# Optimization experiments

Measured on AMD Instinct MI355X. Metric: run time of the kernel, lower is better.

## Reference

```python
import jax, jax.numpy as jnp
import numpy as np

H = 512; W = 512
NUM_CLS = 3; NUM_ANCH = 6; CODE = 7
DIR_BINS = 2; DIR_OFFSET = 0.78539; DIR_LIMIT_OFFSET = 0.0
SCORE_THRESH = 0.1; PRE_K = 4096; POST_K = 500; IOU_THRESH = 0.01
N = H * W * NUM_ANCH  # 1,572,864 anchors


def make_anchors():
    # grid anchors matching [H, W, 3 classes, 2 rotations, 7] layout -> [N, 7]
    xs = jnp.linspace(0.0, 69.12, W, dtype=jnp.float32)
    ys = jnp.linspace(-39.68, 39.68, H, dtype=jnp.float32)
    yy, xx = jnp.meshgrid(ys, xs, indexing='ij')
    cen = jnp.stack([xx, yy, jnp.full_like(xx, -1.0)], -1)  # [H,W,3]
    sizes = jnp.array([[3.9, 1.6, 1.56], [0.8, 0.6, 1.73], [1.76, 0.6, 1.73]], jnp.float32)
    rots = jnp.array([0.0, np.pi / 2], jnp.float32)
    cen = jnp.broadcast_to(cen[:, :, None, None, :], (H, W, 3, 2, 3))
    siz = jnp.broadcast_to(sizes[None, None, :, None, :], (H, W, 3, 2, 3))
    rot = jnp.broadcast_to(rots[None, None, None, :, None], (H, W, 3, 2, 1))
    return jnp.concatenate([cen, siz, rot], -1).reshape(N, CODE)


def setup_inputs() -> dict:
    key = jax.random.key(0)
    k1, k2, k3 = jax.random.split(key, 3)
    return {
        'cls_preds': jax.random.normal(k1, (1, H, W, NUM_ANCH * NUM_CLS), jnp.float32),
        'box_preds': jax.random.normal(k2, (1, H, W, NUM_ANCH * CODE), jnp.float32),
        'dir_cls_preds': jax.random.normal(k3, (1, H, W, NUM_ANCH * DIR_BINS), jnp.float32),
        'anchors': make_anchors(),
    }


def decode_boxes(box_preds, anchors):
    # OpenPCDet ResidualCoder.decode_torch
    xa, ya, za, dxa, dya, dza, ra = [anchors[:, i] for i in range(CODE)]
    xt, yt, zt, dxt, dyt, dzt, rt = [box_preds[:, i] for i in range(CODE)]
    za = za + dza * 0.5
    diag = jnp.sqrt(dxa * dxa + dya * dya)
    xg = xt * diag + xa
    yg = yt * diag + ya
    zg = zt * dza + za
    dxg = jnp.exp(dxt) * dxa
    dyg = jnp.exp(dyt) * dya
    dzg = jnp.exp(dzt) * dza
    rg = rt + ra
    zg = zg - dzg * 0.5
    return jnp.stack([xg, yg, zg, dxg, dyg, dzg, rg], -1)


def reference(cls_preds, box_preds, dir_cls_preds, anchors):
    cls = cls_preds.reshape(N, NUM_CLS)
    box = box_preds.reshape(N, CODE)
    dirp = dir_cls_preds.reshape(N, DIR_BINS)
    boxes = decode_boxes(box, anchors)  # [N,7]
    # direction classifier: limit_period then add bin offset
    dir_labels = jnp.argmax(dirp, -1).astype(jnp.float32)
    period = 2.0 * np.pi / DIR_BINS
    rot = boxes[:, 6]
    val = rot - DIR_OFFSET
    val = val - jnp.floor(val / period + DIR_LIMIT_OFFSET) * period
    rot = val + DIR_OFFSET + period * dir_labels
    boxes = jnp.concatenate([boxes[:, :6], rot[:, None]], -1)
    # post_processing: sigmoid scores, class-agnostic NMS
    probs = jax.nn.sigmoid(cls)
    scores = probs.max(-1)
    labels = probs.argmax(-1) + 1
    scores = jnp.where(scores >= SCORE_THRESH, scores, 0.0)
    top_scores, top_idx = jax.lax.top_k(scores, PRE_K)
    tb = boxes[top_idx]  # [PRE_K,7]
    tl = labels[top_idx]
    # axis-aligned BEV IoU (rotation-agnostic approximation of rotated NMS)
    x1 = tb[:, 0] - tb[:, 3] * 0.5; x2 = tb[:, 0] + tb[:, 3] * 0.5
    y1 = tb[:, 1] - tb[:, 4] * 0.5; y2 = tb[:, 1] + tb[:, 4] * 0.5
    area = (x2 - x1) * (y2 - y1)
    ix = jnp.clip(jnp.minimum(x2[:, None], x2[None, :]) - jnp.maximum(x1[:, None], x1[None, :]), 0.0)
    iy = jnp.clip(jnp.minimum(y2[:, None], y2[None, :]) - jnp.maximum(y1[:, None], y1[None, :]), 0.0)
    inter = ix * iy
    iou = inter / (area[:, None] + area[None, :] - inter + 1e-6)  # [PRE_K,PRE_K]
    valid = top_scores > 0.0
    idxs = jnp.arange(PRE_K)
    def step(keep, i):
        row = iou[i]
        suppressed = jnp.any((row > IOU_THRESH) & keep & (idxs < i))
        ki = valid[i] & jnp.logical_not(suppressed)
        return keep.at[i].set(ki), None
    keep, _ = jax.lax.scan(step, jnp.zeros(PRE_K, bool), idxs)
    final_scores = jnp.where(keep, top_scores, 0.0)
    fs, fi = jax.lax.top_k(final_scores, POST_K)
    out = jnp.concatenate([tb[fi], fs[:, None]], -1)  # [POST_K, 8] boxes+score
    return out, tl[fi]
```

## Files before the change

### kernel.cpp

```cpp
#include <hip/hip_runtime.h>
#include <math.h>

namespace {
constexpr int H = 512, W = 512, NUM_ANCH = 6;
constexpr int N = H * W * NUM_ANCH;
constexpr int NG = N / 4;
constexpr int PREK = 4096;
constexpr int POSTK = 500;
constexpr float SCORE_THRESH = 0.1f;
constexpr float IOU_THRESH = 0.01f;
constexpr float DIR_OFFSET = 0.78539f;
constexpr float PERIOD = 3.14159265358979323846f;
constexpr int LISTB_CAP = 8192;

constexpr size_t oScores = 0;
constexpr size_t oMask   = 0;
constexpr size_t oDiag2  = (size_t)PREK * 64 * 8;
constexpr size_t oHist12 = (size_t)N * 4;
constexpr size_t oHistA  = oHist12 + 4096 * 4;
constexpr size_t oHistB  = oHistA + 1024 * 4;
constexpr size_t oMeta   = oHistB + 1024 * 4;
constexpr size_t oListAS = oMeta + 64 * 4;
constexpr size_t oListAI = oListAS + PREK * 4;
constexpr size_t oListB  = oListAI + PREK * 4;
constexpr size_t oTopS   = oListB + (size_t)LISTB_CAP * 4;
constexpr size_t oTopI   = oTopS + PREK * 4;
constexpr size_t oTB     = oTopI + PREK * 4;
constexpr size_t oB4     = oTB + (size_t)PREK * 7 * 4;
constexpr size_t oLabel  = oB4 + (size_t)PREK * 16;
constexpr size_t oValidW = oLabel + PREK * 4;
constexpr size_t WS_NEED = oValidW + 64 * 8;
}

__device__ __forceinline__ float sigmoid_rn(float x) {
  return (float)(1.0 / (1.0 + exp(-(double)x)));
}

__device__ __forceinline__ unsigned long long rdl64(unsigned long long v, int src) {
  unsigned lo = (unsigned)__builtin_amdgcn_readlane((int)(unsigned)v, src);
  unsigned hi = (unsigned)__builtin_amdgcn_readlane((int)(unsigned)(v >> 32), src);
  return ((unsigned long long)hi << 32) | lo;
}

__device__ __forceinline__ unsigned long long rl2(unsigned lo, unsigned hi, int ln) {
  unsigned a = (unsigned)__builtin_amdgcn_readlane((int)lo, ln);
  unsigned b = (unsigned)__builtin_amdgcn_readlane((int)hi, ln);
  return ((unsigned long long)b << 32) | a;
}

__device__ __forceinline__ void scan_find(const unsigned* __restrict__ hist, int nbins,
                                          unsigned R, unsigned& bin, unsigned& above,
                                          unsigned* part) {
  int t = threadIdx.x;
  int chunk = nbins >> 8;
  unsigned s = 0;
  for (int c = 0; c < chunk; ++c) s += hist[t * chunk + c];
  part[t] = s;
  __syncthreads();
  for (int off = 1; off < 256; off <<= 1) {
    unsigned v = part[t];
    unsigned add = (t + off < 256) ? part[t + off] : 0u;
    __syncthreads();
    part[t] = v + add;
    __syncthreads();
  }
  unsigned cum = (t == 255) ? 0u : part[t + 1];
  for (int c = chunk - 1; c >= 0; --c) {
    unsigned hv = hist[t * chunk + c];
    unsigned ab = cum;
    cum += hv;
    if (cum >= R && ab < R) { part[256] = (unsigned)(t * chunk + c); part[257] = ab; }
  }
  __syncthreads();
  bin = part[256];
  above = part[257];
  __syncthreads();
}

__global__ __launch_bounds__(256) void k_scores(const float4* __restrict__ cls4,
                                                float4* __restrict__ scores4,
                                                unsigned* __restrict__ hist12) {
  __shared__ unsigned h[4096];
  for (int t = threadIdx.x; t < 4096; t += 256) h[t] = 0;
  __syncthreads();
  int stride = gridDim.x * 256;
  for (int g = blockIdx.x * 256 + threadIdx.x; g < NG; g += stride) {
    float4 a = cls4[(size_t)g * 3 + 0];
    float4 b = cls4[(size_t)g * 3 + 1];
    float4 c = cls4[(size_t)g * 3 + 2];
    float m0 = fmaxf(a.x, fmaxf(a.y, a.z));
    float m1 = fmaxf(a.w, fmaxf(b.x, b.y));
    float m2 = fmaxf(b.z, fmaxf(b.w, c.x));
    float m3 = fmaxf(c.y, fmaxf(c.z, c.w));
    float s0 = sigmoid_rn(m0); s0 = (s0 >= SCORE_THRESH) ? s0 : 0.0f;
    float s1 = sigmoid_rn(m1); s1 = (s1 >= SCORE_THRESH) ? s1 : 0.0f;
    float s2 = sigmoid_rn(m2); s2 = (s2 >= SCORE_THRESH) ? s2 : 0.0f;
    float s3 = sigmoid_rn(m3); s3 = (s3 >= SCORE_THRESH) ? s3 : 0.0f;
    scores4[g] = make_float4(s0, s1, s2, s3);
    atomicAdd(&h[__float_as_uint(s0) >> 20], 1u);
    atomicAdd(&h[__float_as_uint(s1) >> 20], 1u);
    atomicAdd(&h[__float_as_uint(s2) >> 20], 1u);
    atomicAdd(&h[__float_as_uint(s3) >> 20], 1u);
  }
  __syncthreads();
  for (int t = threadIdx.x; t < 4096; t += 256) {
    unsigned v = h[t];
    if (v) atomicAdd(&hist12[t], v);
  }
}

__global__ __launch_bounds__(256) void k_refineA(const float4* __restrict__ scores4,
                                                 const unsigned* __restrict__ hist12,
                                                 unsigned* __restrict__ histA,
                                                 unsigned* __restrict__ meta) {
  __shared__ unsigned h[1024];
  __shared__ unsigned part[258];
  for (int t = threadIdx.x; t < 1024; t += 256) h[t] = 0;
  unsigned T1, ab1;
  scan_find(hist12, 4096, PREK, T1, ab1, part);
  if (threadIdx.x == 0) { meta[0] = T1; meta[1] = ab1; }
  int stride = gridDim.x * 256;
  for (int g = blockIdx.x * 256 + threadIdx.x; g < NG; g += stride) {
    float4 s = scores4[g];
    unsigned bb[4] = {__float_as_uint(s.x), __float_as_uint(s.y),
                      __float_as_uint(s.z), __float_as_uint(s.w)};
#pragma unroll
    for (int k = 0; k < 4; ++k)
      if ((bb[k] >> 20) == T1) atomicAdd(&h[(bb[k] >> 10) & 1023u], 1u);
  }
  __syncthreads();
  for (int t = threadIdx.x; t < 1024; t += 256) {
    unsigned v = h[t];
    if (v) atomicAdd(&histA[t], v);
  }
}

__global__ __launch_bounds__(256) void k_refineB(const float4* __restrict__ scores4,
                                                 const unsigned* __restrict__ histA,
                                                 unsigned* __restrict__ histB,
                                                 unsigned* __restrict__ meta) {
  __shared__ unsigned h[1024];
  __shared__ unsigned part[258];
  for (int t = threadIdx.x; t < 1024; t += 256) h[t] = 0;
  unsigned m0 = meta[0], prev = meta[1];
  unsigned T2, ab2;
  scan_find(histA, 1024, PREK - prev, T2, ab2, part);
  if (threadIdx.x == 0) { meta[2] = T2; meta[3] = prev + ab2; }
  unsigned pref22 = (m0 << 10) | T2;
  int stride = gridDim.x * 256;
  for (int g = blockIdx.x * 256 + threadIdx.x; g < NG; g += stride) {
    float4 s = scores4[g];
    unsigned bb[4] = {__float_as_uint(s.x), __float_as_uint(s.y),
                      __float_as_uint(s.z), __float_as_uint(s.w)};
#pragma unroll
    for (int k = 0; k < 4; ++k)
      if ((bb[k] >> 10) == pref22) atomicAdd(&h[bb[k] & 1023u], 1u);
  }
  __syncthreads();
  for (int t = threadIdx.x; t < 1024; t += 256) {
    unsigned v = h[t];
    if (v) atomicAdd(&histB[t], v);
  }
}

__global__ __launch_bounds__(256) void k_compactS(const float4* __restrict__ scores4,
                                                  const unsigned* __restrict__ histB,
                                                  unsigned* __restrict__ meta,
                                                  float* __restrict__ laS,
                                                  unsigned* __restrict__ laI,
                                                  unsigned* __restrict__ lb) {
  __shared__ unsigned part[258];
  unsigned m0 = meta[0], m2 = meta[2], prev = meta[3];
  unsigned R3 = PREK - prev;
  unsigned T3, ab3;
  scan_find(histB, 1024, R3, T3, ab3, part);
  if (threadIdx.x == 0) { meta[12] = T3; meta[6] = R3 - ab3; }
  unsigned thr = (m0 << 20) | (m2 << 10) | T3;
  int stride = gridDim.x * 256;
  for (int g = blockIdx.x * 256 + threadIdx.x; g < NG; g += stride) {
    float4 s = scores4[g];
    float sv[4] = {s.x, s.y, s.z, s.w};
#pragma unroll
    for (int k = 0; k < 4; ++k) {
      unsigned bits = __float_as_uint(sv[k]);
      int n = g * 4 + k;
      if (bits > thr) {
        unsigned pos = atomicAdd(&meta[7], 1u);
        if (pos < (unsigned)PREK) { laS[pos] = sv[k]; laI[pos] = (unsigned)n; }
      } else if (bits == thr) {
        unsigned pos = atomicAdd(&meta[8], 1u);
        if (pos < (unsigned)LISTB_CAP) lb[pos] = (unsigned)n;
      }
    }
  }
}

__global__ __launch_bounds__(1024) void k_select(const unsigned* __restrict__ meta,
                                                 const float* __restrict__ laS,
                                                 const unsigned* __restrict__ laI,
                                                 const unsigned* __restrict__ lb,
                                                 float* __restrict__ topS,
                                                 unsigned* __restrict__ topI,
                                                 unsigned long long* __restrict__ validW) {
  __shared__ unsigned arrB[LISTB_CAP];
  __shared__ unsigned long long arr[PREK];
  int t = threadIdx.x;
  unsigned E = meta[6];
  unsigned G = meta[7];
  unsigned cntB = meta[8];
  if (cntB > (unsigned)LISTB_CAP) cntB = LISTB_CAP;
  unsigned thr = (meta[0] << 20) | (meta[2] << 10) | meta[12];

  if (E != 0) {
    int n2 = 2;
    while ((unsigned)n2 < cntB) n2 <<= 1;
    for (int i = t; i < n2; i += 1024) arrB[i] = (i < (int)cntB) ? lb[i] : 0xFFFFFFFFu;
    __syncthreads();
    if (cntB != E) {
      for (int k = 2; k <= n2; k <<= 1) {
        for (int j = k >> 1; j > 0; j >>= 1) {
          for (int p = t; p < n2 / 2; p += 1024) {
            int i = ((p / j) * (2 * j)) + (p % j);
            int l = i + j;
            bool up = ((i & k) == 0);
            unsigned a = arrB[i], b = arrB[l];
            if ((a > b) == up) { arrB[i] = b; arrB[l] = a; }
          }
          __syncthreads();
        }
      }
    }
    for (int i = t; i < (int)E; i += 1024)
      arr[G + i] = ((unsigned long long)thr << 32) | (unsigned long long)(~arrB[i]);
  }
  __syncthreads();
  for (int i = t; i < PREK; i += 1024)
    if (i < (int)G)
      arr[i] = ((unsigned long long)__float_as_uint(laS[i]) << 32) |
               (unsigned long long)(~laI[i]);
  __syncthreads();
  for (int k = 2; k <= PREK; k <<= 1) {
    for (int j = k >> 1; j > 0; j >>= 1) {
      for (int p = t; p < PREK / 2; p += 1024) {
        int i = ((p / j) * (2 * j)) + (p % j);
        int l = i + j;
        bool up = ((i & k) == 0);
        unsigned long long a = arr[i], b = arr[l];
        if ((a < b) == up) { arr[i] = b; arr[l] = a; }
      }
      __syncthreads();
    }
  }
  for (int i = t; i < PREK; i += 1024) {
    unsigned long long key = arr[i];
    unsigned sb = (unsigned)(key >> 32);
    topS[i] = __uint_as_float(sb);
    topI[i] = ~((unsigned)key);
    unsigned long long bal = __ballot(sb != 0);
    if ((t & 63) == 0) validW[i >> 6] = bal;
  }
}

__global__ void k_decode(const float* __restrict__ cls, const float* __restrict__ box,
                         const float* __restrict__ dir, const float* __restrict__ anc,
                         const unsigned* __restrict__ topI,
                         float* __restrict__ tb, float4* __restrict__ b4,
                         unsigned* __restrict__ label) {
  int i = blockIdx.x * blockDim.x + threadIdx.x;
  if (i >= PREK) return;
  size_t idx = (size_t)topI[i];
  const float* a = anc + idx * 7;
  const float* b = box + idx * 7;
  float xa = a[0], ya = a[1], za = a[2], dxa = a[3], dya = a[4], dza = a[5], ra = a[6];
  float xt = b[0], yt = b[1], zt = b[2], dxt = b[3], dyt = b[4], dzt = b[5], rt = b[6];
  za = za + dza * 0.5f;
  float diagl = sqrtf(dxa * dxa + dya * dya);
  float xg = xt * diagl + xa;
  float yg = yt * diagl + ya;
  float zg = zt * dza + za;
  float dxg = (float)exp((double)dxt) * dxa;
  float dyg = (float)exp((double)dyt) * dya;
  float dzg = (float)exp((double)dzt) * dza;
  float rg = rt + ra;
  zg = zg - dzg * 0.5f;
  float d0 = dir[idx * 2], d1 = dir[idx * 2 + 1];
  float dl = (d1 > d0) ? 1.0f : 0.0f;
  float val = rg - DIR_OFFSET;
  val = val - floorf(val / PERIOD) * PERIOD;
  float rot = val + DIR_OFFSET + PERIOD * dl;
  float l0 = cls[idx * 3 + 0];
  float l1 = cls[idx * 3 + 1];
  float l2 = cls[idx * 3 + 2];
  unsigned lab = 1;
  float bestl = l0;
  if (l1 > bestl) { bestl = l1; lab = 2; }
  if (l2 > bestl) { bestl = l2; lab = 3; }
  tb[i * 7 + 0] = xg; tb[i * 7 + 1] = yg; tb[i * 7 + 2] = zg;
  tb[i * 7 + 3] = dxg; tb[i * 7 + 4] = dyg; tb[i * 7 + 5] = dzg;
  tb[i * 7 + 6] = rot;
  float X1 = xg - dxg * 0.5f, X2 = xg + dxg * 0.5f;
  float Y1 = yg - dyg * 0.5f, Y2 = yg + dyg * 0.5f;
  b4[i] = make_float4(X1, Y1, X2, Y2);
  label[i] = lab;
}

__global__ __launch_bounds__(256) void k_maskgen(const float4* __restrict__ b4,
                                                 unsigned long long* __restrict__ mask,
                                                 unsigned long long* __restrict__ diag2) {
  __shared__ float4 sb[PREK];
  int t = threadIdx.x;
  for (int i = t; i < PREK; i += 256) sb[i] = b4[i];
  __syncthreads();
  int lane = t & 63, wv = t >> 6;
  for (int k = wv; k < 16; k += 4) {
    int r = blockIdx.x + (k << 8);
    float4 bi = sb[r];
    float A = (bi.z - bi.x) * (bi.w - bi.y);
    unsigned long long myword = 0;
    unsigned long long d0 = 0, d1 = 0;
    int w0 = r >> 6;
    int b2 = (r >> 7) << 1;
    for (int w = w0; w < 64; ++w) {
      int j = (w << 6) + lane;
      float4 bj = sb[j];
      float ix = fminf(bi.z, bj.z) - fmaxf(bi.x, bj.x); ix = fmaxf(ix, 0.0f);
      float iy = fminf(bi.w, bj.w) - fmaxf(bi.y, bj.y); iy = fmaxf(iy, 0.0f);
      float inter = ix * iy;
      float Aj = (bj.z - bj.x) * (bj.w - bj.y);
      float iou = inter / (A + Aj - inter + 1e-6f);
      unsigned long long word = __ballot(j > r && iou > IOU_THRESH);
      if (lane == w) myword = word;
      if (w == b2) d0 = word;
      if (w == b2 + 1) d1 = word;
    }
    mask[((size_t)r << 6) + lane] = myword;
    if (lane == 0) {
      unsigned long long* dp = diag2 +
          ((size_t)(r >> 7) * 256 + (size_t)((r >> 6) & 1) * 128 + (size_t)(r & 63) * 2);
      dp[0] = d0; dp[1] = d1;
    }
  }
}

__global__ __launch_bounds__(512) void k_tail(const float* __restrict__ topS,
                                              const float* __restrict__ tb,
                                              const unsigned* __restrict__ label,
                                              const unsigned long long* __restrict__ validW,
                                              const unsigned long long* __restrict__ mask,
                                              const unsigned long long* __restrict__ diag2,
                                              float* __restrict__ out) {
  __shared__ unsigned long long kwS[64];
  __shared__ int part[512];
  __shared__ short keptList[PREK];
  __shared__ short nonKept[PREK];
  int t = threadIdx.x;
  if (t < 64) {
    int lane = t;
    unsigned long long valid_l = validW[lane];
    unsigned long long removed = 0, keep_l = 0;
    const uint4* d4 = (const uint4*)diag2;
    uint4 dA = d4[lane];
    uint4 dB = d4[64 + lane];
    int keptTotal = 0;
    for (int c = 0; c < 32; ++c) {
      uint4 dA1 = dA, dB1 = dB;
      if (c + 1 < 32) {
        dA1 = d4[(c + 1) * 128 + lane];
        dB1 = d4[(c + 1) * 128 + 64 + lane];
      }
      unsigned long long rem0 = rdl64(removed, 2 * c);
      unsigned long long rem1 = rdl64(removed, 2 * c + 1);
      unsigned long long val0 = rdl64(valid_l, 2 * c);
      unsigned long long val1 = rdl64(valid_l, 2 * c + 1);
      unsigned long long p0 = val0 & ~rem0;
      unsigned long long p1 = val1 & ~rem1;
      unsigned long long k0 = 0, k1 = 0;
      while (p0) {
        int b = __ffsll((long long)p0) - 1;
        b = __builtin_amdgcn_readfirstlane(b);
        k0 |= (1ull << b);
        unsigned long long r0 = rl2(dA.x, dA.y, b);
        unsigned long long r1 = rl2(dA.z, dA.w, b);
        p0 &= (p0 - 1);
        p0 &= ~r0;
        p1 &= ~r1;
      }
      while (p1) {
        int b = __ffsll((long long)p1) - 1;
        b = __builtin_amdgcn_readfirstlane(b);
        k1 |= (1ull << b);
        unsigned long long r1 = rl2(dB.z, dB.w, b);
        p1 &= (p1 - 1);
        p1 &= ~r1;
      }
      if (lane == 2 * c) keep_l = k0;
      if (lane == 2 * c + 1) keep_l = k1;
      keptTotal += (int)__popcll(k0) + (int)__popcll(k1);
      if (keptTotal >= POSTK) break;
      unsigned long long kw0 = k0, kw1 = k1;
      size_t rowbase = ((size_t)c << 7);
      while (kw0 | kw1) {
        unsigned long long vv[16];
        unsigned long long mk[16];
#pragma unroll
        for (int u = 0; u < 16; ++u) {
          bool en = ((kw0 | kw1) != 0);
          int b = 0;
          if (kw0) { b = __ffsll((long long)kw0) - 1; kw0 &= kw0 - 1; }
          else if (kw1) { b = 64 + __ffsll((long long)kw1) - 1; kw1 &= kw1 - 1; }
          mk[u] = en ? ~0ull : 0ull;
          vv[u] = mask[((rowbase + (size_t)b) << 6) + lane];
        }
        unsigned long long o = 0;
#pragma unroll
        for (int u = 0; u < 16; ++u) o |= (vv[u] & mk[u]);
        removed |= o;
      }
      dA = dA1;
      dB = dB1;
    }
    kwS[lane] = keep_l;
  }
  __syncthreads();
  int base = t * 8;
  int cnt = 0;
  for (int e = 0; e < 8; ++e) {
    int i = base + e;
    cnt += (int)((kwS[i >> 6] >> (i & 63)) & 1ull);
  }
  part[t] = cnt;
  __syncthreads();
  for (int off = 1; off < 512; off <<= 1) {
    int v = part[t];
    int add = (t >= off) ? part[t - off] : 0;
    __syncthreads();
    part[t] = v + add;
    __syncthreads();
  }
  int kbase = part[t] - cnt;
  int nbase = base - kbase;
  for (int e = 0; e < 8; ++e) {
    int i = base + e;
    bool kp = ((kwS[i >> 6] >> (i & 63)) & 1ull) != 0;
    if (kp) keptList[kbase++] = (short)i;
    else nonKept[nbase++] = (short)i;
  }
  __syncthreads();
  int keptCount = part[511];
  for (int k = t; k < POSTK; k += 512) {
    int i;
    float s;
    if (k < keptCount) { i = keptList[k]; s = topS[i]; }
    else { i = nonKept[k - keptCount]; s = 0.0f; }
    for (int c = 0; c < 7; ++c) out[k * 8 + c] = tb[i * 7 + c];
    out[k * 8 + 7] = s;
    out[POSTK * 8 + k] = (float)label[i];
  }
}

extern "C" void kernel_launch(void* const* d_in, const int* in_sizes, int n_in,
                              void* d_out, int out_size, void* d_ws, size_t ws_size,
                              hipStream_t stream) {
  const float* cls = (const float*)d_in[0];
  const float* box = (const float*)d_in[1];
  const float* dir = (const float*)d_in[2];
  const float* anc = (const float*)d_in[3];
  float* out = (float*)d_out;
  char* ws = (char*)d_ws;
  if (ws_size < WS_NEED) return;

  float* scores = (float*)(ws + oScores);
  unsigned* hist12 = (unsigned*)(ws + oHist12);
  unsigned* histA = (unsigned*)(ws + oHistA);
  unsigned* histB = (unsigned*)(ws + oHistB);
  unsigned* meta = (unsigned*)(ws + oMeta);
  float* laS = (float*)(ws + oListAS);
  unsigned* laI = (unsigned*)(ws + oListAI);
  unsigned* lb = (unsigned*)(ws + oListB);
  float* topS = (float*)(ws + oTopS);
  unsigned* topI = (unsigned*)(ws + oTopI);
  float* tb = (float*)(ws + oTB);
  float4* b4 = (float4*)(ws + oB4);
  unsigned* label = (unsigned*)(ws + oLabel);
  unsigned long long* validW = (unsigned long long*)(ws + oValidW);
  unsigned long long* mask = (unsigned long long*)(ws + oMask);
  unsigned long long* diag2 = (unsigned long long*)(ws + oDiag2);

  hipMemsetAsync(ws + oHist12, 0, (oListAS - oHist12), stream);

  k_scores<<<256, 256, 0, stream>>>((const float4*)cls, (float4*)scores, hist12);
  k_refineA<<<256, 256, 0, stream>>>((const float4*)scores, hist12, histA, meta);
  k_refineB<<<256, 256, 0, stream>>>((const float4*)scores, histA, histB, meta);
  k_compactS<<<256, 256, 0, stream>>>((const float4*)scores, histB, meta, laS, laI, lb);
  k_select<<<1, 1024, 0, stream>>>(meta, laS, laI, lb, topS, topI, validW);
  k_decode<<<PREK / 256, 256, 0, stream>>>(cls, box, dir, anc, topI, tb, b4, label);
  k_maskgen<<<256, 256, 0, stream>>>(b4, mask, diag2);
  k_tail<<<1, 512, 0, stream>>>(topS, tb, label, validW, mask, diag2, out);
}
```

Before: 220.3 us.

## Compact top-bucket candidates once and refine top-k in a single block with fused decode

Replaces two extra full-array histogram passes and a separate compaction with one compaction of all scores in or above the first-level threshold bucket into a 64K candidate buffer. The second and third radix refinement levels, the tie handling and the final sort then run inside one 1024-thread block over that buffer. Box decoding is fused into the same kernel, removing two launches and the topI round trip. The risk is that the candidate bucket may exceed the fixed capacity and the single-block refinement serialises work over many candidates.

```diff
diff --git a/kernel.cpp b/kernel.cpp
--- a/kernel.cpp
+++ b/kernel.cpp
@@ -7,25 +7,22 @@
 constexpr int NG = N / 4;
 constexpr int PREK = 4096;
 constexpr int POSTK = 500;
+constexpr int CAP2 = 65536;
+constexpr int TIEC = 8184;
 constexpr float SCORE_THRESH = 0.1f;
 constexpr float IOU_THRESH = 0.01f;
 constexpr float DIR_OFFSET = 0.78539f;
 constexpr float PERIOD = 3.14159265358979323846f;
-constexpr int LISTB_CAP = 8192;
 
 constexpr size_t oScores = 0;
 constexpr size_t oMask   = 0;
 constexpr size_t oDiag2  = (size_t)PREK * 64 * 8;
 constexpr size_t oHist12 = (size_t)N * 4;
-constexpr size_t oHistA  = oHist12 + 4096 * 4;
-constexpr size_t oHistB  = oHistA + 1024 * 4;
-constexpr size_t oMeta   = oHistB + 1024 * 4;
-constexpr size_t oListAS = oMeta + 64 * 4;
-constexpr size_t oListAI = oListAS + PREK * 4;
-constexpr size_t oListB  = oListAI + PREK * 4;
-constexpr size_t oTopS   = oListB + (size_t)LISTB_CAP * 4;
-constexpr size_t oTopI   = oTopS + PREK * 4;
-constexpr size_t oTB     = oTopI + PREK * 4;
+constexpr size_t oMeta   = oHist12 + 4096 * 4;
+constexpr size_t oCandS  = oMeta + 256;
+constexpr size_t oCandI  = oCandS + (size_t)CAP2 * 4;
+constexpr size_t oTopS   = oCandI + (size_t)CAP2 * 4;
+constexpr size_t oTB     = oTopS + PREK * 4;
 constexpr size_t oB4     = oTB + (size_t)PREK * 7 * 4;
 constexpr size_t oLabel  = oB4 + (size_t)PREK * 16;
 constexpr size_t oValidW = oLabel + PREK * 4;
@@ -109,73 +106,16 @@
   }
 }
 
-__global__ __launch_bounds__(256) void k_refineA(const float4* __restrict__ scores4,
-                                                 const unsigned* __restrict__ hist12,
-                                                 unsigned* __restrict__ histA,
-                                                 unsigned* __restrict__ meta) {
-  __shared__ unsigned h[1024];
+__global__ __launch_bounds__(256) void k_compact2(const float4* __restrict__ scores4,
+                                                  const unsigned* __restrict__ hist12,
+                                                  unsigned* __restrict__ meta,
+                                                  float* __restrict__ caS,
+                                                  unsigned* __restrict__ caI) {
   __shared__ unsigned part[258];
-  for (int t = threadIdx.x; t < 1024; t += 256) h[t] = 0;
   unsigned T1, ab1;
   scan_find(hist12, 4096, PREK, T1, ab1, part);
   if (threadIdx.x == 0) { meta[0] = T1; meta[1] = ab1; }
-  int stride = gridDim.x * 256;
-  for (int g = blockIdx.x * 256 + threadIdx.x; g < NG; g += stride) {
-    float4 s = scores4[g];
-    unsigned bb[4] = {__float_as_uint(s.x), __float_as_uint(s.y),
-                      __float_as_uint(s.z), __float_as_uint(s.w)};
-#pragma unroll
-    for (int k = 0; k < 4; ++k)
-      if ((bb[k] >> 20) == T1) atomicAdd(&h[(bb[k] >> 10) & 1023u], 1u);
-  }
-  __syncthreads();
-  for (int t = threadIdx.x; t < 1024; t += 256) {
-    unsigned v = h[t];
-    if (v) atomicAdd(&histA[t], v);
-  }
-}
-
-__global__ __launch_bounds__(256) void k_refineB(const float4* __restrict__ scores4,
-                                                 const unsigned* __restrict__ histA,
-                                                 unsigned* __restrict__ histB,
-                                                 unsigned* __restrict__ meta) {
-  __shared__ unsigned h[1024];
-  __shared__ unsigned part[258];
-  for (int t = threadIdx.x; t < 1024; t += 256) h[t] = 0;
-  unsigned m0 = meta[0], prev = meta[1];
-  unsigned T2, ab2;
-  scan_find(histA, 1024, PREK - prev, T2, ab2, part);
-  if (threadIdx.x == 0) { meta[2] = T2; meta[3] = prev + ab2; }
-  unsigned pref22 = (m0 << 10) | T2;
-  int stride = gridDim.x * 256;
-  for (int g = blockIdx.x * 256 + threadIdx.x; g < NG; g += stride) {
-    float4 s = scores4[g];
-    unsigned bb[4] = {__float_as_uint(s.x), __float_as_uint(s.y),
-                      __float_as_uint(s.z), __float_as_uint(s.w)};
-#pragma unroll
-    for (int k = 0; k < 4; ++k)
-      if ((bb[k] >> 10) == pref22) atomicAdd(&h[bb[k] & 1023u], 1u);
-  }
-  __syncthreads();
-  for (int t = threadIdx.x; t < 1024; t += 256) {
-    unsigned v = h[t];
-    if (v) atomicAdd(&histB[t], v);
-  }
-}
-
-__global__ __launch_bounds__(256) void k_compactS(const float4* __restrict__ scores4,
-                                                  const unsigned* __restrict__ histB,
-                                                  unsigned* __restrict__ meta,
-                                                  float* __restrict__ laS,
-                                                  unsigned* __restrict__ laI,
-                                                  unsigned* __restrict__ lb) {
-  __shared__ unsigned part[258];
-  unsigned m0 = meta[0], m2 = meta[2], prev = meta[3];
-  unsigned R3 = PREK - prev;
-  unsigned T3, ab3;
-  scan_find(histB, 1024, R3, T3, ab3, part);
-  if (threadIdx.x == 0) { meta[12] = T3; meta[6] = R3 - ab3; }
-  unsigned thr = (m0 << 20) | (m2 << 10) | T3;
+  unsigned lo = T1 << 20;
   int stride = gridDim.x * 256;
   for (int g = blockIdx.x * 256 + threadIdx.x; g < NG; g += stride) {
     float4 s = scores4[g];
@@ -183,40 +123,110 @@
 #pragma unroll
     for (int k = 0; k < 4; ++k) {
       unsigned bits = __float_as_uint(sv[k]);
-      int n = g * 4 + k;
-      if (bits > thr) {
-        unsigned pos = atomicAdd(&meta[7], 1u);
-        if (pos < (unsigned)PREK) { laS[pos] = sv[k]; laI[pos] = (unsigned)n; }
-      } else if (bits == thr) {
-        unsigned pos = atomicAdd(&meta[8], 1u);
-        if (pos < (unsigned)LISTB_CAP) lb[pos] = (unsigned)n;
-      }
-    }
-  }
-}
-
-__global__ __launch_bounds__(1024) void k_select(const unsigned* __restrict__ meta,
-                                                 const float* __restrict__ laS,
-                                                 const unsigned* __restrict__ laI,
-                                                 const unsigned* __restrict__ lb,
-                                                 float* __restrict__ topS,
-                                                 unsigned* __restrict__ topI,
-                                                 unsigned long long* __restrict__ validW) {
-  __shared__ unsigned arrB[LISTB_CAP];
+      if (bits >= lo) {
+        unsigned pos = atomicAdd(&meta[9], 1u);
+        if (pos < (unsigned)CAP2) { caS[pos] = sv[k]; caI[pos] = (unsigned)(g * 4 + k); }
+      }
+    }
+  }
+}
+
+__global__ __launch_bounds__(1024) void k_select2(const unsigned* __restrict__ meta,
+                                                  const float* __restrict__ caS,
+                                                  const unsigned* __restrict__ caI,
+                                                  const float* __restrict__ cls,
+                                                  const float* __restrict__ box,
+                                                  const float* __restrict__ dir,
+                                                  const float* __restrict__ anc,
+                                                  float* __restrict__ topS,
+                                                  unsigned long long* __restrict__ validW,
+                                                  float* __restrict__ tb,
+                                                  float4* __restrict__ b4,
+                                                  unsigned* __restrict__ label) {
   __shared__ unsigned long long arr[PREK];
+  __shared__ unsigned arrB[TIEC];
+  __shared__ unsigned sres[8];
+  unsigned* h = (unsigned*)arr;
+  unsigned* scan = arrB;
   int t = threadIdx.x;
-  unsigned E = meta[6];
-  unsigned G = meta[7];
-  unsigned cntB = meta[8];
-  if (cntB > (unsigned)LISTB_CAP) cntB = LISTB_CAP;
-  unsigned thr = (meta[0] << 20) | (meta[2] << 10) | meta[12];
-
+  unsigned T1 = meta[0], ab1 = meta[1];
+  unsigned cnt2 = meta[9];
+  if (cnt2 > (unsigned)CAP2) cnt2 = CAP2;
+  h[t] = 0;
+  __syncthreads();
+  for (unsigned i = t; i < cnt2; i += 1024) {
+    unsigned bits = __float_as_uint(caS[i]);
+    if ((bits >> 20) == T1) atomicAdd(&h[(bits >> 10) & 1023u], 1u);
+  }
+  __syncthreads();
+  scan[t] = h[t];
+  __syncthreads();
+  for (int off = 1; off < 1024; off <<= 1) {
+    unsigned v = scan[t];
+    unsigned add = (t + off < 1024) ? scan[t + off] : 0u;
+    __syncthreads();
+    scan[t] = v + add;
+    __syncthreads();
+  }
+  unsigned R2 = PREK - ab1;
+  {
+    unsigned cum = scan[t];
+    unsigned ab = (t == 1023) ? 0u : scan[t + 1];
+    if (cum >= R2 && ab < R2) { sres[0] = (unsigned)t; sres[1] = ab; }
+  }
+  __syncthreads();
+  unsigned T2 = sres[0], ab2 = sres[1];
+  __syncthreads();
+  h[t] = 0;
+  __syncthreads();
+  unsigned pref22 = (T1 << 10) | T2;
+  for (unsigned i = t; i < cnt2; i += 1024) {
+    unsigned bits = __float_as_uint(caS[i]);
+    if ((bits >> 10) == pref22) atomicAdd(&h[bits & 1023u], 1u);
+  }
+  __syncthreads();
+  scan[t] = h[t];
+  __syncthreads();
+  for (int off = 1; off < 1024; off <<= 1) {
+    unsigned v = scan[t];
+    unsigned add = (t + off < 1024) ? scan[t + off] : 0u;
+    __syncthreads();
+    scan[t] = v + add;
+    __syncthreads();
+  }
+  unsigned R3 = R2 - ab2;
+  {
+    unsigned cum = scan[t];
+    unsigned ab = (t == 1023) ? 0u : scan[t + 1];
+    if (cum >= R3 && ab < R3) { sres[2] = (unsigned)t; sres[3] = ab; }
+  }
+  __syncthreads();
+  unsigned T3 = sres[2], ab3 = sres[3];
+  unsigned E = R3 - ab3;
+  unsigned thr = (T1 << 20) | (T2 << 10) | T3;
+  if (t == 0) { sres[4] = 0; sres[5] = 0; }
+  __syncthreads();
+  for (unsigned i = t; i < cnt2; i += 1024) {
+    unsigned bits = __float_as_uint(caS[i]);
+    if (bits > thr) {
+      unsigned pos = atomicAdd(&sres[4], 1u);
+      arr[pos] = ((unsigned long long)bits << 32) | (unsigned long long)(~caI[i]);
+    } else if (bits == thr) {
+      unsigned pos = atomicAdd(&sres[5], 1u);
+      if (pos < (unsigned)TIEC) arrB[pos] = caI[i];
+    }
+  }
+  __syncthreads();
+  unsigned G = sres[4];
+  unsigned cntB = sres[5];
+  if (cntB > (unsigned)TIEC) cntB = TIEC;
   if (E != 0) {
-    int n2 = 2;
-    while ((unsigned)n2 < cntB) n2 <<= 1;
-    for (int i = t; i < n2; i += 1024) arrB[i] = (i < (int)cntB) ? lb[i] : 0xFFFFFFFFu;
-    __syncthreads();
     if (cntB != E) {
+      int n2 = 2;
+      while ((unsigned)n2 < cntB) n2 <<= 1;
+      for (int i = t; i < n2; i += 1024)
+        if (i >= (int)cntB) arrB[i] = 0xFFFFFFFFu;
+      __syncthreads();
       for (int k = 2; k <= n2; k <<= 1) {
         for (int j = k >> 1; j > 0; j >>= 1) {
           for (int p = t; p < n2 / 2; p += 1024) {
@@ -234,11 +244,6 @@
       arr[G + i] = ((unsigned long long)thr << 32) | (unsigned long long)(~arrB[i]);
   }
   __syncthreads();
-  for (int i = t; i < PREK; i += 1024)
-    if (i < (int)G)
-      arr[i] = ((unsigned long long)__float_as_uint(laS[i]) << 32) |
-               (unsigned long long)(~laI[i]);
-  __syncthreads();
   for (int k = 2; k <= PREK; k <<= 1) {
     for (int j = k >> 1; j > 0; j >>= 1) {
       for (int p = t; p < PREK / 2; p += 1024) {
@@ -255,53 +260,43 @@
     unsigned long long key = arr[i];
     unsigned sb = (unsigned)(key >> 32);
     topS[i] = __uint_as_float(sb);
-    topI[i] = ~((unsigned)key);
     unsigned long long bal = __ballot(sb != 0);
     if ((t & 63) == 0) validW[i >> 6] = bal;
-  }
-}
-
-__global__ void k_decode(const float* __restrict__ cls, const float* __restrict__ box,
-                         const float* __restrict__ dir, const float* __restrict__ anc,
-                         const unsigned* __restrict__ topI,
-                         float* __restrict__ tb, float4* __restrict__ b4,
-                         unsigned* __restrict__ label) {
-  int i = blockIdx.x * blockDim.x + threadIdx.x;
-  if (i >= PREK) return;
-  size_t idx = (size_t)topI[i];
-  const float* a = anc + idx * 7;
-  const float* b = box + idx * 7;
-  float xa = a[0], ya = a[1], za = a[2], dxa = a[3], dya = a[4], dza = a[5], ra = a[6];
-  float xt = b[0], yt = b[1], zt = b[2], dxt = b[3], dyt = b[4], dzt = b[5], rt = b[6];
-  za = za + dza * 0.5f;
-  float diagl = sqrtf(dxa * dxa + dya * dya);
-  float xg = xt * diagl + xa;
-  float yg = yt * diagl + ya;
-  float zg = zt * dza + za;
-  float dxg = (float)exp((double)dxt) * dxa;
-  float dyg = (float)exp((double)dyt) * dya;
-  float dzg = (float)exp((double)dzt) * dza;
-  float rg = rt + ra;
-  zg = zg - dzg * 0.5f;
-  float d0 = dir[idx * 2], d1 = dir[idx * 2 + 1];
-  float dl = (d1 > d0) ? 1.0f : 0.0f;
-  float val = rg - DIR_OFFSET;
-  val = val - floorf(val / PERIOD) * PERIOD;
-  float rot = val + DIR_OFFSET + PERIOD * dl;
-  float l0 = cls[idx * 3 + 0];
-  float l1 = cls[idx * 3 + 1];
-  float l2 = cls[idx * 3 + 2];
-  unsigned lab = 1;
-  float bestl = l0;
-  if (l1 > bestl) { bestl = l1; lab = 2; }
-  if (l2 > bestl) { bestl = l2; lab = 3; }
-  tb[i * 7 + 0] = xg; tb[i * 7 + 1] = yg; tb[i * 7 + 2] = zg;
-  tb[i * 7 + 3] = dxg; tb[i * 7 + 4] = dyg; tb[i * 7 + 5] = dzg;
-  tb[i * 7 + 6] = rot;
-  float X1 = xg - dxg * 0.5f, X2 = xg + dxg * 0.5f;
-  float Y1 = yg - dyg * 0.5f, Y2 = yg + dyg * 0.5f;
-  b4[i] = make_float4(X1, Y1, X2, Y2);
-  label[i] = lab;
+    size_t idx = (size_t)(~((unsigned)key));
+    const float* a = anc + idx * 7;
+    const float* b = box + idx * 7;
+    float xa = a[0], ya = a[1], za = a[2], dxa = a[3], dya = a[4], dza = a[5], ra = a[6];
+    float xt = b[0], yt = b[1], zt = b[2], dxt = b[3], dyt = b[4], dzt = b[5], rt = b[6];
+    za = za + dza * 0.5f;
+    float diagl = sqrtf(dxa * dxa + dya * dya);
+    float xg = xt * diagl + xa;
+    float yg = yt * diagl + ya;
+    float zg = zt * dza + za;
+    float dxg = (float)exp((double)dxt) * dxa;
+    float dyg = (float)exp((double)dyt) * dya;
+    float dzg = (float)exp((double)dzt) * dza;
+    float rg = rt + ra;
+    zg = zg - dzg * 0.5f;
+    float d0 = dir[idx * 2], d1 = dir[idx * 2 + 1];
+    float dl = (d1 > d0) ? 1.0f : 0.0f;
+    float val = rg - DIR_OFFSET;
+    val = val - floorf(val / PERIOD) * PERIOD;
+    float rot = val + DIR_OFFSET + PERIOD * dl;
+    float l0 = cls[idx * 3 + 0];
+    float l1 = cls[idx * 3 + 1];
+    float l2 = cls[idx * 3 + 2];
+    unsigned lab = 1;
+    float bestl = l0;
+    if (l1 > bestl) { bestl = l1; lab = 2; }
+    if (l2 > bestl) { bestl = l2; lab = 3; }
+    tb[i * 7 + 0] = xg; tb[i * 7 + 1] = yg; tb[i * 7 + 2] = zg;
+    tb[i * 7 + 3] = dxg; tb[i * 7 + 4] = dyg; tb[i * 7 + 5] = dzg;
+    tb[i * 7 + 6] = rot;
+    float X1 = xg - dxg * 0.5f, X2 = xg + dxg * 0.5f;
+    float Y1 = yg - dyg * 0.5f, Y2 = yg + dyg * 0.5f;
+    b4[i] = make_float4(X1, Y1, X2, Y2);
+    label[i] = lab;
+  }
 }
 
 __global__ __launch_bounds__(256) void k_maskgen(const float4* __restrict__ b4,
@@ -471,14 +466,10 @@
 
   float* scores = (float*)(ws + oScores);
   unsigned* hist12 = (unsigned*)(ws + oHist12);
-  unsigned* histA = (unsigned*)(ws + oHistA);
-  unsigned* histB = (unsigned*)(ws + oHistB);
   unsigned* meta = (unsigned*)(ws + oMeta);
-  float* laS = (float*)(ws + oListAS);
-  unsigned* laI = (unsigned*)(ws + oListAI);
-  unsigned* lb = (unsigned*)(ws + oListB);
+  float* caS = (float*)(ws + oCandS);
+  unsigned* caI = (unsigned*)(ws + oCandI);
   float* topS = (float*)(ws + oTopS);
-  unsigned* topI = (unsigned*)(ws + oTopI);
   float* tb = (float*)(ws + oTB);
   float4* b4 = (float4*)(ws + oB4);
   unsigned* label = (unsigned*)(ws + oLabel);
@@ -486,14 +477,12 @@
   unsigned long long* mask = (unsigned long long*)(ws + oMask);
   unsigned long long* diag2 = (unsigned long long*)(ws + oDiag2);
 
-  hipMemsetAsync(ws + oHist12, 0, (oListAS - oHist12), stream);
+  hipMemsetAsync(ws + oHist12, 0, (oCandS - oHist12), stream);
 
   k_scores<<<256, 256, 0, stream>>>((const float4*)cls, (float4*)scores, hist12);
-  k_refineA<<<256, 256, 0, stream>>>((const float4*)scores, hist12, histA, meta);
-  k_refineB<<<256, 256, 0, stream>>>((const float4*)scores, histA, histB, meta);
-  k_compactS<<<256, 256, 0, stream>>>((const float4*)scores, histB, meta, laS, laI, lb);
-  k_select<<<1, 1024, 0, stream>>>(meta, laS, laI, lb, topS, topI, validW);
-  k_decode<<<PREK / 256, 256, 0, stream>>>(cls, box, dir, anc, topI, tb, b4, label);
+  k_compact2<<<256, 256, 0, stream>>>((const float4*)scores, hist12, meta, caS, caI);
+  k_select2<<<1, 1024, 0, stream>>>(meta, caS, caI, cls, box, dir, anc,
+                                    topS, validW, tb, b4, label);
   k_maskgen<<<256, 256, 0, stream>>>(b4, mask, diag2);
   k_tail<<<1, 512, 0, stream>>>(topS, tb, label, validW, mask, diag2, out);
 }
```

Result: slower. 342.2 us (+55.4%).

## Fuse radix-select passes into one persistent kernel with grid barriers; fold decode into select

Applied to the files above, without the earlier changes.

The four score/histogram/refine/compact kernels are merged into one persistent kernel of 256 blocks that uses a software grid barrier (atomic counter plus phase flag) between the radix-select passes. The thresholds now stay in registers instead of being handed through meta. The separate decode kernel is folded into the single-block select kernel, which drops the topI buffer and two launches. The intent is to remove kernel launch gaps and global round trips. The cost is that the barrier relies on all 256 blocks being co-resident, and decode now runs on a single block instead of 16.

```diff
diff --git a/kernel.cpp b/kernel.cpp
--- a/kernel.cpp
+++ b/kernel.cpp
@@ -7,6 +7,7 @@
 constexpr int NG = N / 4;
 constexpr int PREK = 4096;
 constexpr int POSTK = 500;
+constexpr int FBLK = 256;
 constexpr float SCORE_THRESH = 0.1f;
 constexpr float IOU_THRESH = 0.01f;
 constexpr float DIR_OFFSET = 0.78539f;
@@ -24,8 +25,7 @@
 constexpr size_t oListAI = oListAS + PREK * 4;
 constexpr size_t oListB  = oListAI + PREK * 4;
 constexpr size_t oTopS   = oListB + (size_t)LISTB_CAP * 4;
-constexpr size_t oTopI   = oTopS + PREK * 4;
-constexpr size_t oTB     = oTopI + PREK * 4;
+constexpr size_t oTB     = oTopS + PREK * 4;
 constexpr size_t oB4     = oTB + (size_t)PREK * 7 * 4;
 constexpr size_t oLabel  = oB4 + (size_t)PREK * 16;
 constexpr size_t oValidW = oLabel + PREK * 4;
@@ -46,6 +46,22 @@
   unsigned a = (unsigned)__builtin_amdgcn_readlane((int)lo, ln);
   unsigned b = (unsigned)__builtin_amdgcn_readlane((int)hi, ln);
   return ((unsigned long long)b << 32) | a;
+}
+
+__device__ __forceinline__ void grid_bar(unsigned* cnt, unsigned* phase, unsigned tgt) {
+  __syncthreads();
+  if (threadIdx.x == 0) {
+    unsigned my = __hip_atomic_fetch_add(cnt, 1u, __ATOMIC_ACQ_REL,
+                                         __HIP_MEMORY_SCOPE_AGENT);
+    if (my == (unsigned)(FBLK - 1)) {
+      __hip_atomic_store(cnt, 0u, __ATOMIC_RELAXED, __HIP_MEMORY_SCOPE_AGENT);
+      __hip_atomic_fetch_add(phase, 1u, __ATOMIC_RELEASE, __HIP_MEMORY_SCOPE_AGENT);
+    } else {
+      while (__hip_atomic_load(phase, __ATOMIC_ACQUIRE, __HIP_MEMORY_SCOPE_AGENT) < tgt)
+        __builtin_amdgcn_s_sleep(8);
+    }
+  }
+  __syncthreads();
 }
 
 __device__ __forceinline__ void scan_find(const unsigned* __restrict__ hist, int nbins,
@@ -77,14 +93,24 @@
   __syncthreads();
 }
 
-__global__ __launch_bounds__(256) void k_scores(const float4* __restrict__ cls4,
-                                                float4* __restrict__ scores4,
-                                                unsigned* __restrict__ hist12) {
+__global__ __launch_bounds__(256) void k_front(const float4* __restrict__ cls4,
+                                               float4* __restrict__ scores4,
+                                               unsigned* __restrict__ hist12,
+                                               unsigned* __restrict__ histA,
+                                               unsigned* __restrict__ histB,
+                                               unsigned* __restrict__ meta,
+                                               float* __restrict__ laS,
+                                               unsigned* __restrict__ laI,
+                                               unsigned* __restrict__ lb) {
   __shared__ unsigned h[4096];
-  for (int t = threadIdx.x; t < 4096; t += 256) h[t] = 0;
-  __syncthreads();
-  int stride = gridDim.x * 256;
-  for (int g = blockIdx.x * 256 + threadIdx.x; g < NG; g += stride) {
+  __shared__ unsigned part[258];
+  unsigned* barC = &meta[16];
+  unsigned* barP = &meta[17];
+  int t = threadIdx.x;
+  int stride = FBLK * 256;
+  for (int i = t; i < 4096; i += 256) h[i] = 0;
+  __syncthreads();
+  for (int g = blockIdx.x * 256 + t; g < NG; g += stride) {
     float4 a = cls4[(size_t)g * 3 + 0];
     float4 b = cls4[(size_t)g * 3 + 1];
     float4 c = cls4[(size_t)g * 3 + 2];
@@ -103,24 +129,16 @@
     atomicAdd(&h[__float_as_uint(s3) >> 20], 1u);
   }
   __syncthreads();
-  for (int t = threadIdx.x; t < 4096; t += 256) {
-    unsigned v = h[t];
-    if (v) atomicAdd(&hist12[t], v);
-  }
-}
-
-__global__ __launch_bounds__(256) void k_refineA(const float4* __restrict__ scores4,
-                                                 const unsigned* __restrict__ hist12,
-                                                 unsigned* __restrict__ histA,
-                                                 unsigned* __restrict__ meta) {
-  __shared__ unsigned h[1024];
-  __shared__ unsigned part[258];
-  for (int t = threadIdx.x; t < 1024; t += 256) h[t] = 0;
+  for (int i = t; i < 4096; i += 256) {
+    unsigned v = h[i];
+    if (v) atomicAdd(&hist12[i], v);
+  }
+  grid_bar(barC, barP, 1);
   unsigned T1, ab1;
   scan_find(hist12, 4096, PREK, T1, ab1, part);
-  if (threadIdx.x == 0) { meta[0] = T1; meta[1] = ab1; }
-  int stride = gridDim.x * 256;
-  for (int g = blockIdx.x * 256 + threadIdx.x; g < NG; g += stride) {
+  for (int i = t; i < 1024; i += 256) h[i] = 0;
+  __syncthreads();
+  for (int g = blockIdx.x * 256 + t; g < NG; g += stride) {
     float4 s = scores4[g];
     unsigned bb[4] = {__float_as_uint(s.x), __float_as_uint(s.y),
                       __float_as_uint(s.z), __float_as_uint(s.w)};
@@ -129,26 +147,17 @@
       if ((bb[k] >> 20) == T1) atomicAdd(&h[(bb[k] >> 10) & 1023u], 1u);
   }
   __syncthreads();
-  for (int t = threadIdx.x; t < 1024; t += 256) {
-    unsigned v = h[t];
-    if (v) atomicAdd(&histA[t], v);
-  }
-}
-
-__global__ __launch_bounds__(256) void k_refineB(const float4* __restrict__ scores4,
-                                                 const unsigned* __restrict__ histA,
-                                                 unsigned* __restrict__ histB,
-                                                 unsigned* __restrict__ meta) {
-  __shared__ unsigned h[1024];
-  __shared__ unsigned part[258];
-  for (int t = threadIdx.x; t < 1024; t += 256) h[t] = 0;
-  unsigned m0 = meta[0], prev = meta[1];
+  for (int i = t; i < 1024; i += 256) {
+    unsigned v = h[i];
+    if (v) atomicAdd(&histA[i], v);
+  }
+  grid_bar(barC, barP, 2);
   unsigned T2, ab2;
-  scan_find(histA, 1024, PREK - prev, T2, ab2, part);
-  if (threadIdx.x == 0) { meta[2] = T2; meta[3] = prev + ab2; }
-  unsigned pref22 = (m0 << 10) | T2;
-  int stride = gridDim.x * 256;
-  for (int g = blockIdx.x * 256 + threadIdx.x; g < NG; g += stride) {
+  scan_find(histA, 1024, PREK - ab1, T2, ab2, part);
+  unsigned pref22 = (T1 << 10) | T2;
+  for (int i = t; i < 1024; i += 256) h[i] = 0;
+  __syncthreads();
+  for (int g = blockIdx.x * 256 + t; g < NG; g += stride) {
     float4 s = scores4[g];
     unsigned bb[4] = {__float_as_uint(s.x), __float_as_uint(s.y),
                       __float_as_uint(s.z), __float_as_uint(s.w)};
@@ -157,27 +166,19 @@
       if ((bb[k] >> 10) == pref22) atomicAdd(&h[bb[k] & 1023u], 1u);
   }
   __syncthreads();
-  for (int t = threadIdx.x; t < 1024; t += 256) {
-    unsigned v = h[t];
-    if (v) atomicAdd(&histB[t], v);
-  }
-}
-
-__global__ __launch_bounds__(256) void k_compactS(const float4* __restrict__ scores4,
-                                                  const unsigned* __restrict__ histB,
-                                                  unsigned* __restrict__ meta,
-                                                  float* __restrict__ laS,
-                                                  unsigned* __restrict__ laI,
-                                                  unsigned* __restrict__ lb) {
-  __shared__ unsigned part[258];
-  unsigned m0 = meta[0], m2 = meta[2], prev = meta[3];
-  unsigned R3 = PREK - prev;
+  for (int i = t; i < 1024; i += 256) {
+    unsigned v = h[i];
+    if (v) atomicAdd(&histB[i], v);
+  }
+  grid_bar(barC, barP, 3);
+  unsigned R3 = PREK - ab1 - ab2;
   unsigned T3, ab3;
   scan_find(histB, 1024, R3, T3, ab3, part);
-  if (threadIdx.x == 0) { meta[12] = T3; meta[6] = R3 - ab3; }
-  unsigned thr = (m0 << 20) | (m2 << 10) | T3;
-  int stride = gridDim.x * 256;
-  for (int g = blockIdx.x * 256 + threadIdx.x; g < NG; g += stride) {
+  if (t == 0) {
+    meta[0] = T1; meta[2] = T2; meta[12] = T3; meta[6] = R3 - ab3;
+  }
+  unsigned thr = (T1 << 20) | (T2 << 10) | T3;
+  for (int g = blockIdx.x * 256 + t; g < NG; g += stride) {
     float4 s = scores4[g];
     float sv[4] = {s.x, s.y, s.z, s.w};
 #pragma unroll
@@ -195,13 +196,19 @@
   }
 }
 
-__global__ __launch_bounds__(1024) void k_select(const unsigned* __restrict__ meta,
-                                                 const float* __restrict__ laS,
-                                                 const unsigned* __restrict__ laI,
-                                                 const unsigned* __restrict__ lb,
-                                                 float* __restrict__ topS,
-                                                 unsigned* __restrict__ topI,
-                                                 unsigned long long* __restrict__ validW) {
+__global__ __launch_bounds__(1024) void k_selectdec(const unsigned* __restrict__ meta,
+                                                    const float* __restrict__ laS,
+                                                    const unsigned* __restrict__ laI,
+                                                    const unsigned* __restrict__ lb,
+                                                    const float* __restrict__ cls,
+                                                    const float* __restrict__ box,
+                                                    const float* __restrict__ dir,
+                                                    const float* __restrict__ anc,
+                                                    float* __restrict__ topS,
+                                                    unsigned long long* __restrict__ validW,
+                                                    float* __restrict__ tb,
+                                                    float4* __restrict__ b4,
+                                                    unsigned* __restrict__ label) {
   __shared__ unsigned arrB[LISTB_CAP];
   __shared__ unsigned long long arr[PREK];
   int t = threadIdx.x;
@@ -255,53 +262,43 @@
     unsigned long long key = arr[i];
     unsigned sb = (unsigned)(key >> 32);
     topS[i] = __uint_as_float(sb);
-    topI[i] = ~((unsigned)key);
     unsigned long long bal = __ballot(sb != 0);
     if ((t & 63) == 0) validW[i >> 6] = bal;
-  }
-}
-
-__global__ void k_decode(const float* __restrict__ cls, const float* __restrict__ box,
-                         const float* __restrict__ dir, const float* __restrict__ anc,
-                         const unsigned* __restrict__ topI,
-                         float* __restrict__ tb, float4* __restrict__ b4,
-                         unsigned* __restrict__ label) {
-  int i = blockIdx.x * blockDim.x + threadIdx.x;
-  if (i >= PREK) return;
-  size_t idx = (size_t)topI[i];
-  const float* a = anc + idx * 7;
-  const float* b = box + idx * 7;
-  float xa = a[0], ya = a[1], za = a[2], dxa = a[3], dya = a[4], dza = a[5], ra = a[6];
-  float xt = b[0], yt = b[1], zt = b[2], dxt = b[3], dyt = b[4], dzt = b[5], rt = b[6];
-  za = za + dza * 0.5f;
-  float diagl = sqrtf(dxa * dxa + dya * dya);
-  float xg = xt * diagl + xa;
-  float yg = yt * diagl + ya;
-  float zg = zt * dza + za;
-  float dxg = (float)exp((double)dxt) * dxa;
-  float dyg = (float)exp((double)dyt) * dya;
-  float dzg = (float)exp((double)dzt) * dza;
-  float rg = rt + ra;
-  zg = zg - dzg * 0.5f;
-  float d0 = dir[idx * 2], d1 = dir[idx * 2 + 1];
-  float dl = (d1 > d0) ? 1.0f : 0.0f;
-  float val = rg - DIR_OFFSET;
-  val = val - floorf(val / PERIOD) * PERIOD;
-  float rot = val + DIR_OFFSET + PERIOD * dl;
-  float l0 = cls[idx * 3 + 0];
-  float l1 = cls[idx * 3 + 1];
-  float l2 = cls[idx * 3 + 2];
-  unsigned lab = 1;
-  float bestl = l0;
-  if (l1 > bestl) { bestl = l1; lab = 2; }
-  if (l2 > bestl) { bestl = l2; lab = 3; }
-  tb[i * 7 + 0] = xg; tb[i * 7 + 1] = yg; tb[i * 7 + 2] = zg;
-  tb[i * 7 + 3] = dxg; tb[i * 7 + 4] = dyg; tb[i * 7 + 5] = dzg;
-  tb[i * 7 + 6] = rot;
-  float X1 = xg - dxg * 0.5f, X2 = xg + dxg * 0.5f;
-  float Y1 = yg - dyg * 0.5f, Y2 = yg + dyg * 0.5f;
-  b4[i] = make_float4(X1, Y1, X2, Y2);
-  label[i] = lab;
+    size_t idx = (size_t)(~((unsigned)key));
+    const float* a = anc + idx * 7;
+    const float* b = box + idx * 7;
+    float xa = a[0], ya = a[1], za = a[2], dxa = a[3], dya = a[4], dza = a[5], ra = a[6];
+    float xt = b[0], yt = b[1], zt = b[2], dxt = b[3], dyt = b[4], dzt = b[5], rt = b[6];
+    za = za + dza * 0.5f;
+    float diagl = sqrtf(dxa * dxa + dya * dya);
+    float xg = xt * diagl + xa;
+    float yg = yt * diagl + ya;
+    float zg = zt * dza + za;
+    float dxg = (float)exp((double)dxt) * dxa;
+    float dyg = (float)exp((double)dyt) * dya;
+    float dzg = (float)exp((double)dzt) * dza;
+    float rg = rt + ra;
+    zg = zg - dzg * 0.5f;
+    float d0 = dir[idx * 2], d1 = dir[idx * 2 + 1];
+    float dl = (d1 > d0) ? 1.0f : 0.0f;
+    float val = rg - DIR_OFFSET;
+    val = val - floorf(val / PERIOD) * PERIOD;
+    float rot = val + DIR_OFFSET + PERIOD * dl;
+    float l0 = cls[idx * 3 + 0];
+    float l1 = cls[idx * 3 + 1];
+    float l2 = cls[idx * 3 + 2];
+    unsigned lab = 1;
+    float bestl = l0;
+    if (l1 > bestl) { bestl = l1; lab = 2; }
+    if (l2 > bestl) { bestl = l2; lab = 3; }
+    tb[i * 7 + 0] = xg; tb[i * 7 + 1] = yg; tb[i * 7 + 2] = zg;
+    tb[i * 7 + 3] = dxg; tb[i * 7 + 4] = dyg; tb[i * 7 + 5] = dzg;
+    tb[i * 7 + 6] = rot;
+    float X1 = xg - dxg * 0.5f, X2 = xg + dxg * 0.5f;
+    float Y1 = yg - dyg * 0.5f, Y2 = yg + dyg * 0.5f;
+    b4[i] = make_float4(X1, Y1, X2, Y2);
+    label[i] = lab;
+  }
 }
 
 __global__ __launch_bounds__(256) void k_maskgen(const float4* __restrict__ b4,
@@ -478,7 +475,6 @@
   unsigned* laI = (unsigned*)(ws + oListAI);
   unsigned* lb = (unsigned*)(ws + oListB);
   float* topS = (float*)(ws + oTopS);
-  unsigned* topI = (unsigned*)(ws + oTopI);
   float* tb = (float*)(ws + oTB);
   float4* b4 = (float4*)(ws + oB4);
   unsigned* label = (unsigned*)(ws + oLabel);
@@ -488,12 +484,10 @@
 
   hipMemsetAsync(ws + oHist12, 0, (oListAS - oHist12), stream);
 
-  k_scores<<<256, 256, 0, stream>>>((const float4*)cls, (float4*)scores, hist12);
-  k_refineA<<<256, 256, 0, stream>>>((const float4*)scores, hist12, histA, meta);
-  k_refineB<<<256, 256, 0, stream>>>((const float4*)scores, histA, histB, meta);
-  k_compactS<<<256, 256, 0, stream>>>((const float4*)scores, histB, meta, laS, laI, lb);
-  k_select<<<1, 1024, 0, stream>>>(meta, laS, laI, lb, topS, topI, validW);
-  k_decode<<<PREK / 256, 256, 0, stream>>>(cls, box, dir, anc, topI, tb, b4, label);
+  k_front<<<FBLK, 256, 0, stream>>>((const float4*)cls, (float4*)scores,
+                                    hist12, histA, histB, meta, laS, laI, lb);
+  k_selectdec<<<1, 1024, 0, stream>>>(meta, laS, laI, lb, cls, box, dir, anc,
+                                      topS, validW, tb, b4, label);
   k_maskgen<<<256, 256, 0, stream>>>(b4, mask, diag2);
   k_tail<<<1, 512, 0, stream>>>(topS, tb, label, validW, mask, diag2, out);
 }
```

After: 304.5 us. 1.38x slower.
